# Performance work log

Hardware: AMD Instinct MI355X
Metric: run time of the kernel (lower is better)

The kernel has to match this reference:

```python
import jax, jax.numpy as jnp
import numpy as np

NO_EDGE_OFFSET_T_NORM = 2.0    # pushes no_edge above data range so min() ignores it
NO_EDGE_OFFSET_T_CONORM = -1.0 # pushes no_edge below data range so max() ignores it


def _daa_layer(x, sel, is_t_norm):
    """One DAALayer with a single operator for all nodes (LAYER_WISE init).

    x:   [B, in_features] float
    sel: [out_features, in_features] int, edge type per (node, input):
         0 = no_edge (value 0 + operator-dependent offset), 1 = normal_edge (value x)
    """
    off = NO_EDGE_OFFSET_T_NORM if is_t_norm else NO_EDGE_OFFSET_T_CONORM
    # [B, out, in]: gather edge values per node according to hard routing
    vals = jnp.where(sel[None, :, :] == 1, x[:, None, :], jnp.float32(off))
    # t-norm 'min' / t-conorm 'max' reduction over incoming edges
    return vals.min(axis=-1) if is_t_norm else vals.max(axis=-1)


def setup_inputs() -> dict:
    key = jax.random.key(0)
    k1, k2, k3 = jax.random.split(key, 3)
    B, IN, HID = 256, 1024, 512
    x = jax.random.uniform(k1, (B, IN), dtype=jnp.float32)
    # hard gumbel-softmax over all-ones logits == uniform edge-type choice
    sel0 = jax.random.randint(k2, (HID, IN), 0, 2)  # layer 0: 1024 -> 512
    sel1 = jax.random.randint(k3, (IN, HID), 0, 2)  # layer 1: 512 -> 1024
    return {"x": x, "sel0": sel0, "sel1": sel1}


def reference(x, sel0, sel1):
    h = _daa_layer(x, sel0, True)    # layer 0: T_Norm.min on all nodes
    out = _daa_layer(h, sel1, False)  # layer 1: T_Conorm.max on all nodes
    return out
```

## Files before the change

kernel.cpp:

```cpp
#include <hip/hip_runtime.h>


#define NB 256

__global__ __launch_bounds__(256) void pack_x(
    const float* __restrict__ in, float4* __restrict__ outT4)
{
    __shared__ float t[64][65];
    const int bx = blockIdx.x % 16;
    const int by = blockIdx.x / 16;
    const int i0 = bx * 64, b0 = by * 64;

    const int li = threadIdx.x & 63;
    const int lb = threadIdx.x >> 6;
#pragma unroll
    for (int r = 0; r < 64; r += 4)
        t[lb + r][li] = in[(size_t)(b0 + lb + r) * 1024 + i0 + li];
    __syncthreads();

    const int sb = threadIdx.x & 63;
    const int si = threadIdx.x >> 6;
#pragma unroll
    for (int p = 0; p < 16; p += 4) {
        const int i4 = si + p;
        float4 v = make_float4(t[sb][4 * i4 + 0], t[sb][4 * i4 + 1],
                               t[sb][4 * i4 + 2], t[sb][4 * i4 + 3]);
        outT4[(size_t)(i0 / 4 + i4) * NB + b0 + sb] = v;
    }
}

template<int INF, int OT, int S, bool ISMIN, bool TOUT>
__global__ __launch_bounds__(64 * S, 8) void daa_layer(
    const float4* __restrict__ inT4,
    const int* __restrict__ sel,
    float* __restrict__ out, int OUTF)
{
    constexpr int C4  = INF / 4 / S;
    constexpr int NI4 = OT * INF / 4;
    const int tid  = threadIdx.x;
    const int lane = tid & 63;
    const int s    = __builtin_amdgcn_readfirstlane(tid >> 6);
    const int bch  = blockIdx.x & 1;
    const int o0   = (blockIdx.x >> 1) * OT;
    const int bA   = bch * 128 + lane;
    const float off = ISMIN ? 2.0f : -1.0f;
    const float inf = ISMIN ? __builtin_inff() : -__builtin_inff();

    __shared__ float4 aLDS[NI4];
    if (tid < NI4) {
        const int4 v = ((const int4*)(sel + (size_t)o0 * INF))[tid];
        aLDS[tid] = make_float4(v.x ? 0.f : inf, v.y ? 0.f : inf,
                                v.z ? 0.f : inf, v.w ? 0.f : inf);
    }
    __syncthreads();

    float acc[OT][2];
#pragma unroll
    for (int u = 0; u < OT; ++u) acc[u][0] = acc[u][1] = off;

    const float4* __restrict__ xp = inT4 + (size_t)(s * C4) * NB + bA;

#define MM(A, X, AV)                                                   \
    do {                                                               \
        if (ISMIN) {                                                   \
            A = fminf(fminf(A, (X).x + (AV).x), (X).y + (AV).y);       \
            A = fminf(fminf(A, (X).z + (AV).z), (X).w + (AV).w);       \
        } else {                                                       \
            A = fmaxf(fmaxf(A, (X).x + (AV).x), (X).y + (AV).y);       \
            A = fmaxf(fmaxf(A, (X).z + (AV).z), (X).w + (AV).w);       \
        }                                                              \
    } while (0)

    float4 xa = xp[0], xb = xp[64];
    for (int c = 0; c < C4; ++c) {
        float4 na, nb;
        if (c + 1 < C4) {
            na = xp[(size_t)(c + 1) * NB];
            nb = xp[(size_t)(c + 1) * NB + 64];
        }
#pragma unroll
        for (int u = 0; u < OT; ++u) {
            const float4 av = aLDS[u * (INF / 4) + s * C4 + c];
            MM(acc[u][0], xa, av);
            MM(acc[u][1], xb, av);
        }
        xa = na; xb = nb;
    }
#undef MM

    __shared__ float red[S][OT][2][64];
#pragma unroll
    for (int u = 0; u < OT; ++u)
#pragma unroll
        for (int v = 0; v < 2; ++v) red[s][u][v][lane] = acc[u][v];
    __syncthreads();

    if (tid < 128) {
        const int v  = tid >> 6;
        const int ln = tid & 63;
        const int b  = bch * 128 + v * 64 + ln;
        float r[OT];
#pragma unroll
        for (int u = 0; u < OT; ++u) {
            float q = red[0][u][v][ln];
#pragma unroll
            for (int ss = 1; ss < S; ++ss) {
                const float w = red[ss][u][v][ln];
                q = ISMIN ? fminf(q, w) : fmaxf(q, w);
            }
            r[u] = q;
        }
        static_assert(OT == 4, "float4 store assumes OT==4");
        const float4 o4 = make_float4(r[0], r[1], r[2], r[3]);
        if (TOUT)
            ((float4*)out)[(size_t)(o0 >> 2) * NB + b] = o4;
        else
            *(float4*)(out + (size_t)b * OUTF + o0) = o4;
    }
}

extern "C" void kernel_launch(void* const* d_in, const int* in_sizes, int n_in,
                              void* d_out, int out_size, void* d_ws, size_t ws_size,
                              hipStream_t stream) {
    const float* x    = (const float*)d_in[0];
    const int*   sel0 = (const int*)d_in[1];
    const int*   sel1 = (const int*)d_in[2];
    float* out = (float*)d_out;

    float4* xT4 = (float4*)d_ws;
    float*  hT  = (float*)((char*)d_ws + (1 << 20));

    pack_x<<<64, 256, 0, stream>>>(x, xT4);
    daa_layer<1024, 4, 16, true,  true ><<<256, 1024, 0, stream>>>(
        xT4, sel0, hT, 512);
    daa_layer< 512, 4, 16, false, false><<<512, 1024, 0, stream>>>(
        (const float4*)hT, sel1, out, 1024);
}
```

Baseline: 26.26 us.

## Widen per-block output tile to 8 nodes with half of routing masks precomputed globally

The packing kernel now also converts the selection masks into additive 0/inf float offsets for the upper half of each 8-node group and writes them to workspace. Each layer block now handles 8 output nodes and 64 batch rows instead of 4 nodes and 128 rows. Four node masks come from LDS and the other four are read straight from the precomputed global buffer. This is meant to cut LDS pressure and reuse each x load across more nodes, at the cost of extra global mask reads, a larger pack kernel and an extra reduction stage with more barriers.

```diff
diff --git a/kernel.cpp b/kernel.cpp
--- a/kernel.cpp
+++ b/kernel.cpp
@@ -3,62 +3,88 @@
 
 #define NB 256
 
-__global__ __launch_bounds__(256) void pack_x(
-    const float* __restrict__ in, float4* __restrict__ outT4)
+__global__ __launch_bounds__(256) void pack_all(
+    const float* __restrict__ x,    float4* __restrict__ xT4,
+    const int*   __restrict__ sel0, float4* __restrict__ a0h,
+    const int*   __restrict__ sel1, float4* __restrict__ a1h)
 {
-    __shared__ float t[64][65];
-    const int bx = blockIdx.x % 16;
-    const int by = blockIdx.x / 16;
-    const int i0 = bx * 64, b0 = by * 64;
+    const int t = blockIdx.x * 256 + threadIdx.x;
+    const float pinf = __builtin_inff();
 
-    const int li = threadIdx.x & 63;
-    const int lb = threadIdx.x >> 6;
+    {
+        const int j = t >> 8, i4 = t & 255;
+        const int srow = (j >> 2) * 8 + 4 + (j & 3);
+        const int4 v = ((const int4*)sel0)[srow * 256 + i4];
+        a0h[t] = make_float4(v.x ? 0.f : pinf, v.y ? 0.f : pinf,
+                             v.z ? 0.f : pinf, v.w ? 0.f : pinf);
+    }
+    {
+        const int j = t >> 7, i4 = t & 127;
+        const int srow = (j >> 2) * 8 + 4 + (j & 3);
+        const int4 v = ((const int4*)sel1)[srow * 128 + i4];
+        a1h[t] = make_float4(v.x ? 0.f : -pinf, v.y ? 0.f : -pinf,
+                             v.z ? 0.f : -pinf, v.w ? 0.f : -pinf);
+    }
+
+    if (blockIdx.x < 64) {
+        __shared__ float tt[64][65];
+        const int bx = blockIdx.x % 16;
+        const int by = blockIdx.x / 16;
+        const int i0 = bx * 64, b0 = by * 64;
+
+        const int li = threadIdx.x & 63;
+        const int lb = threadIdx.x >> 6;
 #pragma unroll
-    for (int r = 0; r < 64; r += 4)
-        t[lb + r][li] = in[(size_t)(b0 + lb + r) * 1024 + i0 + li];
-    __syncthreads();
+        for (int r = 0; r < 64; r += 4)
+            tt[lb + r][li] = x[(size_t)(b0 + lb + r) * 1024 + i0 + li];
+        __syncthreads();
 
-    const int sb = threadIdx.x & 63;
-    const int si = threadIdx.x >> 6;
+        const int sb = threadIdx.x & 63;
+        const int si = threadIdx.x >> 6;
 #pragma unroll
-    for (int p = 0; p < 16; p += 4) {
-        const int i4 = si + p;
-        float4 v = make_float4(t[sb][4 * i4 + 0], t[sb][4 * i4 + 1],
-                               t[sb][4 * i4 + 2], t[sb][4 * i4 + 3]);
-        outT4[(size_t)(i0 / 4 + i4) * NB + b0 + sb] = v;
+        for (int p = 0; p < 16; p += 4) {
+            const int i4 = si + p;
+            float4 v = make_float4(tt[sb][4 * i4 + 0], tt[sb][4 * i4 + 1],
+                                   tt[sb][4 * i4 + 2], tt[sb][4 * i4 + 3]);
+            xT4[(size_t)(i0 / 4 + i4) * NB + b0 + sb] = v;
+        }
     }
 }
 
-template<int INF, int OT, int S, bool ISMIN, bool TOUT>
-__global__ __launch_bounds__(64 * S, 8) void daa_layer(
+template<int INF, int S, int MW, bool ISMIN, bool TOUT>
+__global__ __launch_bounds__(64 * S, MW) void daa_layer(
     const float4* __restrict__ inT4,
-    const int* __restrict__ sel,
+    const int*    __restrict__ sel,
+    const float4* __restrict__ agh,
     float* __restrict__ out, int OUTF)
 {
     constexpr int C4  = INF / 4 / S;
-    constexpr int NI4 = OT * INF / 4;
+    constexpr int R4  = INF / 4;
     const int tid  = threadIdx.x;
     const int lane = tid & 63;
     const int s    = __builtin_amdgcn_readfirstlane(tid >> 6);
-    const int bch  = blockIdx.x & 1;
-    const int o0   = (blockIdx.x >> 1) * OT;
-    const int bA   = bch * 128 + lane;
+    const int bch  = blockIdx.x & 3;
+    const int o0   = (blockIdx.x >> 2) * 8;
+    const int b    = bch * 64 + lane;
     const float off = ISMIN ? 2.0f : -1.0f;
     const float inf = ISMIN ? __builtin_inff() : -__builtin_inff();
 
-    __shared__ float4 aLDS[NI4];
-    if (tid < NI4) {
-        const int4 v = ((const int4*)(sel + (size_t)o0 * INF))[tid];
-        aLDS[tid] = make_float4(v.x ? 0.f : inf, v.y ? 0.f : inf,
-                                v.z ? 0.f : inf, v.w ? 0.f : inf);
+    __shared__ float4 uni[2048];
+
+    if (tid < 4 * R4) {
+        const int4 v = ((const int4*)sel)[(size_t)o0 * R4 + tid];
+        uni[tid] = make_float4(v.x ? 0.f : inf, v.y ? 0.f : inf,
+                               v.z ? 0.f : inf, v.w ? 0.f : inf);
     }
     __syncthreads();
 
-    float acc[OT][2];
+    float acc[8];
 #pragma unroll
-    for (int u = 0; u < OT; ++u) acc[u][0] = acc[u][1] = off;
+    for (int u = 0; u < 8; ++u) acc[u] = off;
 
-    const float4* __restrict__ xp = inT4 + (size_t)(s * C4) * NB + bA;
+    const float4* __restrict__ xp = inT4 + (size_t)(s * C4) * NB + b;
+    const float4* __restrict__ aL = uni + s * C4;
+    const float4* __restrict__ aG = agh + ((size_t)(o0 >> 3) * 4) * R4 + s * C4;
 
 #define MM(A, X, AV)                                                   \
     do {                                                               \
@@ -71,51 +97,55 @@
         }                                                              \
     } while (0)
 
-    float4 xa = xp[0], xb = xp[64];
+    float4 xa = xp[0];
     for (int c = 0; c < C4; ++c) {
-        float4 na, nb;
-        if (c + 1 < C4) {
-            na = xp[(size_t)(c + 1) * NB];
-            nb = xp[(size_t)(c + 1) * NB + 64];
+        float4 nx = xa;
+        if (c + 1 < C4) nx = xp[(size_t)(c + 1) * NB];
+#pragma unroll
+        for (int u = 0; u < 4; ++u) {
+            const float4 av = aL[u * R4 + c];
+            MM(acc[u], xa, av);
         }
 #pragma unroll
-        for (int u = 0; u < OT; ++u) {
-            const float4 av = aLDS[u * (INF / 4) + s * C4 + c];
-            MM(acc[u][0], xa, av);
-            MM(acc[u][1], xb, av);
+        for (int u = 0; u < 4; ++u) {
+            const float4 av = aG[u * R4 + c];
+            MM(acc[4 + u], xa, av);
         }
-        xa = na; xb = nb;
+        xa = nx;
     }
 #undef MM
 
-    __shared__ float red[S][OT][2][64];
+    __syncthreads();
+    float* redf = (float*)uni;
 #pragma unroll
-    for (int u = 0; u < OT; ++u)
-#pragma unroll
-        for (int v = 0; v < 2; ++v) red[s][u][v][lane] = acc[u][v];
+    for (int u = 0; u < 8; ++u) redf[(s * 8 + u) * 64 + lane] = acc[u];
     __syncthreads();
 
-    if (tid < 128) {
-        const int v  = tid >> 6;
-        const int ln = tid & 63;
-        const int b  = bch * 128 + v * 64 + ln;
-        float r[OT];
+    if (tid < 512) {
+        const int u = tid >> 6, ln = tid & 63;
+        float v = redf[u * 64 + ln];
 #pragma unroll
-        for (int u = 0; u < OT; ++u) {
-            float q = red[0][u][v][ln];
-#pragma unroll
-            for (int ss = 1; ss < S; ++ss) {
-                const float w = red[ss][u][v][ln];
-                q = ISMIN ? fminf(q, w) : fmaxf(q, w);
-            }
-            r[u] = q;
+        for (int ss = 1; ss < S; ++ss) {
+            const float q = redf[(ss * 8 + u) * 64 + ln];
+            v = ISMIN ? fminf(v, q) : fmaxf(v, q);
         }
-        static_assert(OT == 4, "float4 store assumes OT==4");
-        const float4 o4 = make_float4(r[0], r[1], r[2], r[3]);
-        if (TOUT)
-            ((float4*)out)[(size_t)(o0 >> 2) * NB + b] = o4;
-        else
-            *(float4*)(out + (size_t)b * OUTF + o0) = o4;
+        redf[u * 64 + ln] = v;
+    }
+    __syncthreads();
+
+    if (tid < 64) {
+        const int bb = bch * 64 + tid;
+        const float4 lo = make_float4(redf[0 * 64 + tid], redf[1 * 64 + tid],
+                                      redf[2 * 64 + tid], redf[3 * 64 + tid]);
+        const float4 hi = make_float4(redf[4 * 64 + tid], redf[5 * 64 + tid],
+                                      redf[6 * 64 + tid], redf[7 * 64 + tid]);
+        if (TOUT) {
+            ((float4*)out)[(size_t)(o0 >> 2) * NB + bb]       = lo;
+            ((float4*)out)[((size_t)(o0 >> 2) + 1) * NB + bb] = hi;
+        } else {
+            float4* p = (float4*)(out + (size_t)bb * OUTF + o0);
+            p[0] = lo; p[1] = hi;
+        }
     }
 }
 
@@ -127,12 +157,15 @@
     const int*   sel1 = (const int*)d_in[2];
     float* out = (float*)d_out;
 
-    float4* xT4 = (float4*)d_ws;
-    float*  hT  = (float*)((char*)d_ws + (1 << 20));
+    char* ws = (char*)d_ws;
+    float4* xT4 = (float4*)ws;
+    float*  hT  = (float*)(ws + (1 << 20));
+    float4* a0h = (float4*)(ws + 3 * (1 << 19));
+    float4* a1h = (float4*)(ws + 5 * (1 << 19));
 
-    pack_x<<<64, 256, 0, stream>>>(x, xT4);
-    daa_layer<1024, 4, 16, true,  true ><<<256, 1024, 0, stream>>>(
-        xT4, sel0, hT, 512);
-    daa_layer< 512, 4, 16, false, false><<<512, 1024, 0, stream>>>(
-        (const float4*)hT, sel1, out, 1024);
+    pack_all<<<256, 256, 0, stream>>>(x, xT4, sel0, a0h, sel1, a1h);
+    daa_layer<1024, 16, 4, true,  true ><<<256, 1024, 0, stream>>>(
+        xT4, sel0, a0h, hT, 512);
+    daa_layer< 512, 16, 8, false, false><<<512, 1024, 0, stream>>>(
+        (const float4*)hT, sel1, a1h, out, 1024);
 }
```

Result: faster. 25.35 us (-3.5%).
